# Kernel optimization log

Hardware: AMD Instinct MI355X
Metric: run time of the kernel (lower is better)

Reference implementation:

```python
import jax, jax.numpy as jnp
import numpy as np
import math

B, C, N, M = 4, 128, 4096, 4096

def setup_inputs() -> dict:
    key = jax.random.key(0)
    ks = jax.random.split(key, 8)
    return {
        "x1": jax.random.normal(ks[0], (B, C, N), dtype=jnp.float32),
        "p1": jax.random.normal(ks[1], (B, 3, N), dtype=jnp.float32),
        "x2": jax.random.normal(ks[2], (B, C, M), dtype=jnp.float32),
        "p2": jax.random.normal(ks[3], (B, 3, M), dtype=jnp.float32),
        "Wq": jax.random.normal(ks[4], (C, C), dtype=jnp.float32) * 0.05,
        "Wk": jax.random.normal(ks[5], (C, C), dtype=jnp.float32) * 0.05,
        "Wv": jax.random.normal(ks[6], (C, C), dtype=jnp.float32) * 0.05,
        "Wpos": jax.random.normal(ks[7], (C, 3), dtype=jnp.float32) * 0.05,
    }

def reference(x1, p1, x2, p2, Wq, Wk, Wv, Wpos):
    # Conv1d with kernel_size=1, no bias == per-point matmul over channel dim.
    # NOTE: original forward uses self.pos for BOTH p1 and p2 (pos1 conv unused).
    pos = jnp.einsum('ck,bkn->bcn', Wpos, p1)   # [B,C,N]
    pos1 = jnp.einsum('ck,bkm->bcm', Wpos, p2)  # [B,C,M]
    q = jnp.einsum('dc,bcn->bdn', Wq, x1 + pos)   # [B,C,N]
    k = jnp.einsum('dc,bcm->bdm', Wk, x2 + pos1)  # [B,C,M]
    v = jnp.einsum('dc,bcm->bdm', Wv, x2)         # [B,C,M]
    scale = math.sqrt(q.shape[1])  # sqrt(C) -- q.shape[-2] in (B,C,N) layout
    energy = jnp.einsum('bcn,bcm->bnm', q, k) / scale  # [B,N,M]
    attention = jax.nn.softmax(energy, axis=-1)
    vout = jnp.einsum('bnm,bcm->bnc', attention, v)    # [B,N,C]
    out = jnp.swapaxes(vout, 1, 2) + x1                # [B,C,N] residual
    return jnp.swapaxes(out, 1, 2)                     # [B,N,C]
```

## Files before the change

kernel.cpp:

```cpp
#include <hip/hip_runtime.h>
#include <hip/hip_bf16.h>

#define B_ 4
#define C_ 128
#define N_ 4096
#define M_ 4096

typedef __bf16 bf16;
typedef __bf16 bf16x8 __attribute__((ext_vector_type(8)));
typedef float f32x4 __attribute__((ext_vector_type(4)));
typedef float f32x16 __attribute__((ext_vector_type(16)));

#define MFMA16(a, b, c) __builtin_amdgcn_mfma_f32_16x16x32_bf16(a, b, c, 0, 0, 0)
#define MFMA32(a, b, c) __builtin_amdgcn_mfma_f32_32x32x16_bf16(a, b, c, 0, 0, 0)

__device__ inline void gll16(const bf16* g, bf16* l) {
    __builtin_amdgcn_global_load_lds(
        (const __attribute__((address_space(1))) void*)g,
        (__attribute__((address_space(3))) void*)l, 16, 0, 0);
}

__device__ inline unsigned cvtpk(float a, float b) {
    unsigned r;
    asm("v_cvt_pk_bf16_f32 %0, %1, %2" : "=v"(r) : "v"(a), "v"(b));
    return r;
}

__global__ __launch_bounds__(256) void wcvt_kernel(
    const float* __restrict__ Wq, const float* __restrict__ Wk,
    const float* __restrict__ Wv, bf16* __restrict__ Wb) {
    int i = (blockIdx.x * 256 + threadIdx.x) * 4;
    const float* src = (i < 16384) ? Wq : (i < 32768) ? Wk : Wv;
    int off = i & 16383;
    float4 v = *(const float4*)(src + off);
    union { ushort4 u4; bf16 h[4]; } pk;
    pk.h[0] = (bf16)v.x; pk.h[1] = (bf16)v.y;
    pk.h[2] = (bf16)v.z; pk.h[3] = (bf16)v.w;
    *(ushort4*)(Wb + i) = pk.u4;
}

__global__ __launch_bounds__(256) void proj_kernel(
    const float* __restrict__ x1, const float* __restrict__ p1,
    const float* __restrict__ x2, const float* __restrict__ p2,
    const bf16* __restrict__ Wb, const float* __restrict__ Wpos,
    bf16* __restrict__ Qt, bf16* __restrict__ Kt, bf16* __restrict__ Vt) {
    __shared__ __align__(16) bf16 xt[64 * 136];
    __shared__ float pp[3 * 64], wls[384];

    const int t = threadIdx.x;
    const int b = blockIdx.y;
    const int role = blockIdx.z;
    const int n0 = blockIdx.x * 64;

    const float* xs = (role == 0) ? x1 : x2;
    const float* ps = (role == 0) ? p1 : p2;

    if (role < 2) {
        if (t < 48) {
            int k3 = t / 16, i4 = (t & 15) * 4;
            *(float4*)&pp[k3 * 64 + i4] =
                *(const float4*)(ps + ((size_t)b * 3 + k3) * N_ + n0 + i4);
        } else if (t < 144) {
            int i4 = (t - 48) * 4;
            *(float4*)&wls[i4] = *(const float4*)(Wpos + i4);
        }
    }
    __syncthreads();

    #pragma unroll
    for (int k = 0; k < 8; ++k) {
        int s = t + k * 256;
        int c = s >> 4, n4 = (s & 15) * 4;
        float4 xv = *(const float4*)(xs + ((size_t)b * C_ + c) * N_ + n0 + n4);
        const float* xa = &xv.x;
        if (role < 2) {
            float w0 = wls[c * 3 + 0], w1 = wls[c * 3 + 1], w2 = wls[c * 3 + 2];
            #pragma unroll
            for (int j = 0; j < 4; ++j) {
                float pos = w0 * pp[n4 + j] + w1 * pp[64 + n4 + j] + w2 * pp[128 + n4 + j];
                xt[(n4 + j) * 136 + c] = (bf16)(xa[j] + pos);
            }
        } else {
            #pragma unroll
            for (int j = 0; j < 4; ++j)
                xt[(n4 + j) * 136 + c] = (bf16)xa[j];
        }
    }
    __syncthreads();

    const int w = t >> 6;
    const int lane = t & 63;
    const int col = lane & 15, quad = lane >> 4;
    const int nl = w * 16 + col;

    const bf16* Wm = Wb + role * 16384;

    bf16x8 bx[4];
    #pragma unroll
    for (int cs = 0; cs < 4; ++cs)
        bx[cs] = *(const bf16x8*)&xt[nl * 136 + cs * 32 + quad * 8];

    if (role < 2) {
        bf16* Ot = (role == 0) ? Qt : Kt;
        #pragma unroll
        for (int dt = 0; dt < 8; ++dt) {
            f32x4 acc = {0.f, 0.f, 0.f, 0.f};
            #pragma unroll
            for (int cs = 0; cs < 4; ++cs) {
                bf16x8 wf = *(const bf16x8*)(Wm + (dt * 16 + col) * 128 + cs * 32 + quad * 8);
                acc = MFMA16(bx[cs], wf, acc);
            }
            #pragma unroll
            for (int r = 0; r < 4; ++r) {
                int n = n0 + w * 16 + quad * 4 + r;
                Ot[((size_t)b * N_ + n) * C_ + dt * 16 + col] = (bf16)acc[r];
            }
        }
    } else {
        #pragma unroll
        for (int dt = 0; dt < 8; ++dt) {
            f32x4 acc = {0.f, 0.f, 0.f, 0.f};
            #pragma unroll
            for (int cs = 0; cs < 4; ++cs) {
                bf16x8 wf = *(const bf16x8*)(Wm + (dt * 16 + col) * 128 + cs * 32 + quad * 8);
                acc = MFMA16(wf, bx[cs], acc);
            }
            #pragma unroll
            for (int r = 0; r < 4; ++r)
                Vt[((size_t)b * C_ + dt * 16 + quad * 4 + r) * (size_t)M_ + n0 + nl] = (bf16)acc[r];
        }
    }
}

__global__ __launch_bounds__(512) void attn_kernel(
    const bf16* __restrict__ Qt, const bf16* __restrict__ Kt,
    const bf16* __restrict__ Vt, const float* __restrict__ x1,
    float* __restrict__ out) {
    __shared__ __align__(16) char smem[132096];

    const int t = threadIdx.x;
    const int w = t >> 6;
    const int lane = t & 63;
    const int col = lane & 31;
    const int hi = lane >> 5;
    const int kg = w & 3;
    const int qg = w >> 2;

    const int g0 = blockIdx.x;
    const int xcd = g0 & 7;
    const int b = xcd >> 1;
    const int qt = (xcd & 1) + ((g0 >> 3) << 1);
    const int n0 = qt * 64;

    const float KS = 0.12752107168406815f;

    const bf16* Kbase = Kt + (size_t)b * M_ * C_;
    const bf16* Vbase = Vt + (size_t)b * C_ * M_;

    bf16x8 qf[8];
    {
        const bf16* Qb = Qt + ((size_t)b * N_ + n0 + qg * 32 + col) * C_ + hi * 8;
        #pragma unroll
        for (int cs = 0; cs < 8; ++cs)
            qf[cs] = *(const bf16x8*)(Qb + cs * 16);
    }

    f32x16 oacc[4];
    #pragma unroll
    for (int i = 0; i < 4; ++i)
        #pragma unroll
        for (int j = 0; j < 16; ++j) oacc[i][j] = 0.f;
    float lacc = 0.f;

    const int key_l = (kg << 5) + col;
    const int kxor = (key_l & 15) << 4;

    const bf16* kpp[4];
    const bf16* vpp[4];
    #pragma unroll
    for (int i = 0; i < 4; ++i) {
        int g = ((w << 2) + i) * 64 + lane;
        int row = g >> 4;
        int sp = (g & 15) ^ (row & 15);
        kpp[i] = Kbase + (size_t)row * C_ + sp * 8;
        vpp[i] = Vbase + (size_t)row * M_ + sp * 8;
    }

    auto stageK = [&](char* dst) {
        #pragma unroll
        for (int i = 0; i < 4; ++i) {
            gll16(kpp[i], (bf16*)dst + ((w << 2) + i) * 512);
            kpp[i] += 128 * C_;
        }
    };
    auto stageV = [&](char* dst) {
        #pragma unroll
        for (int i = 0; i < 4; ++i) {
            gll16(vpp[i], (bf16*)dst + ((w << 2) + i) * 512);
            vpp[i] += 128;
        }
    };

    stageK(smem);
    stageV(smem + 65536);
    stageK(smem + 32768);

    f32x16 sA0, sA1, sB0, sB1;

    auto qkc = [&](const char* kbBuf, f32x16& T0, f32x16& T1) {
        #pragma unroll
        for (int q = 0; q < 16; ++q) { T0[q] = 0.f; T1[q] = 0.f; }
        const char* kbp = kbBuf + key_l * 256;
        __builtin_amdgcn_s_setprio(1);
        #pragma unroll
        for (int cs = 0; cs < 4; ++cs) {
            bf16x8 kf = *(const bf16x8*)(kbp + ((((cs << 1) + hi) << 4) ^ kxor));
            T0 = MFMA32(kf, qf[cs], T0);
        }
        #pragma unroll
        for (int cs = 4; cs < 8; ++cs) {
            bf16x8 kf = *(const bf16x8*)(kbp + ((((cs << 1) + hi) << 4) ^ kxor));
            T1 = MFMA32(kf, qf[cs], T1);
        }
        __builtin_amdgcn_s_setprio(0);
    };

    auto smpv = [&](f32x16& S0, f32x16& S1, const char* vbBuf) {
        float p[16];
        #pragma unroll
        for (int r = 0; r < 16; ++r) {
            float e = fminf((S0[r] + S1[r]) * KS, 60.f);
            p[r] = __builtin_amdgcn_exp2f(e);
        }
        {
            float s01 = (p[0] + p[1]) + (p[2] + p[3]);
            float s23 = (p[4] + p[5]) + (p[6] + p[7]);
            float s45 = (p[8] + p[9]) + (p[10] + p[11]);
            float s67 = (p[12] + p[13]) + (p[14] + p[15]);
            lacc += (s01 + s23) + (s45 + s67);
        }
        unsigned W0 = cvtpk(p[0], p[1]),  W1 = cvtpk(p[2], p[3]);
        unsigned W2 = cvtpk(p[4], p[5]),  W3 = cvtpk(p[6], p[7]);
        unsigned W4 = cvtpk(p[8], p[9]),  W5 = cvtpk(p[10], p[11]);
        unsigned W6 = cvtpk(p[12], p[13]), W7 = cvtpk(p[14], p[15]);
        unsigned X0 = hi ? W0 : W2, X1 = hi ? W1 : W3;
        unsigned Y0 = hi ? W4 : W6, Y1 = hi ? W5 : W7;
        X0 = __shfl_xor(X0, 32, 64);  X1 = __shfl_xor(X1, 32, 64);
        Y0 = __shfl_xor(Y0, 32, 64);  Y1 = __shfl_xor(Y1, 32, 64);
        uint4 u0, u1;
        u0.x = hi ? X0 : W0;  u0.y = hi ? X1 : W1;
        u0.z = hi ? W2 : X0;  u0.w = hi ? W3 : X1;
        u1.x = hi ? Y0 : W4;  u1.y = hi ? Y1 : W5;
        u1.z = hi ? W6 : Y0;  u1.w = hi ? W7 : Y1;
        bf16x8 af0 = __builtin_bit_cast(bf16x8, u0);
        bf16x8 af1 = __builtin_bit_cast(bf16x8, u1);

        __builtin_amdgcn_s_setprio(1);
        #pragma unroll
        for (int ct = 0; ct < 4; ++ct) {
            int c = (ct << 5) + col;
            const char* vbp = vbBuf + c * 256;
            int vxor = (c & 15) << 4;
            bf16x8 vf0 = *(const bf16x8*)(vbp + ((((kg << 2) + hi) << 4) ^ vxor));
            bf16x8 vf1 = *(const bf16x8*)(vbp + ((((kg << 2) + 2 + hi) << 4) ^ vxor));
            oacc[ct] = MFMA32(af0, vf0, oacc[ct]);
            oacc[ct] = MFMA32(af1, vf1, oacc[ct]);
        }
        __builtin_amdgcn_s_setprio(0);
    };

    asm volatile("s_waitcnt vmcnt(8)" ::: "memory");
    __builtin_amdgcn_sched_barrier(0);
    __builtin_amdgcn_s_barrier();
    __builtin_amdgcn_sched_barrier(0);
    qkc(smem, sA0, sA1);

    for (int jp = 0; jp < 16; ++jp) {
        const int j0 = jp * 2, j1 = j0 + 1;

        asm volatile("s_waitcnt vmcnt(0)" ::: "memory");
        __builtin_amdgcn_sched_barrier(0);
        __builtin_amdgcn_s_barrier();
        __builtin_amdgcn_sched_barrier(0);
        if (j0 < 31) stageV(smem + 98304);
        if (j0 < 30) stageK(smem);
        if (j0 < 31) qkc(smem + 32768, sB0, sB1);
        smpv(sA0, sA1, smem + 65536);
        asm volatile("s_waitcnt lgkmcnt(0)" ::: "memory");
        __builtin_amdgcn_sched_barrier(0);

        asm volatile("s_waitcnt vmcnt(0)" ::: "memory");
        __builtin_amdgcn_sched_barrier(0);
        __builtin_amdgcn_s_barrier();
        __builtin_amdgcn_sched_barrier(0);
        if (j1 < 31) stageV(smem + 65536);
        if (j1 < 30) stageK(smem + 32768);
        if (j1 < 31) qkc(smem, sA0, sA1);
        smpv(sB0, sB1, smem + 98304);
        asm volatile("s_waitcnt lgkmcnt(0)" ::: "memory");
        __builtin_amdgcn_sched_barrier(0);
    }

    __builtin_amdgcn_s_barrier();

    float* obuf = (float*)smem;
    float* lps  = (float*)(smem + 131072);

    lacc += __shfl_xor(lacc, 32, 64);
    if (hi == 0) lps[(kg << 6) + (qg << 5) + col] = lacc;

    #pragma unroll
    for (int ct = 0; ct < 4; ++ct)
        #pragma unroll
        for (int r = 0; r < 16; ++r) {
            int q = (r & 3) + ((r >> 2) << 3) + (hi << 2);
            obuf[kg * 8192 + ((qg << 5) + q) * 128 + (ct << 5) + col] = oacc[ct][r];
        }
    __syncthreads();

    const int c2 = lane << 1;
    #pragma unroll
    for (int j = 0; j < 8; ++j) {
        int q = (w << 3) + j;
        float s0 = 0.f, s1 = 0.f;
        #pragma unroll
        for (int pp = 0; pp < 4; ++pp) {
            float2 v = *(const float2*)&obuf[pp * 8192 + q * 128 + c2];
            s0 += v.x; s1 += v.y;
        }
        float lsum = lps[q] + lps[64 + q] + lps[128 + q] + lps[192 + q];
        float linv = 1.0f / lsum;
        int n = n0 + q;
        float o0 = s0 * linv + x1[((size_t)b * C_ + c2) * N_ + n];
        float o1 = s1 * linv + x1[((size_t)b * C_ + c2 + 1) * N_ + n];
        *(float2*)&out[((size_t)b * N_ + n) * C_ + c2] = make_float2(o0, o1);
    }
}

extern "C" void kernel_launch(void* const* d_in, const int* in_sizes, int n_in,
                              void* d_out, int out_size, void* d_ws, size_t ws_size,
                              hipStream_t stream) {
    const float* x1   = (const float*)d_in[0];
    const float* p1   = (const float*)d_in[1];
    const float* x2   = (const float*)d_in[2];
    const float* p2   = (const float*)d_in[3];
    const float* Wq   = (const float*)d_in[4];
    const float* Wk   = (const float*)d_in[5];
    const float* Wv   = (const float*)d_in[6];
    const float* Wpos = (const float*)d_in[7];
    float* out = (float*)d_out;

    bf16* Qt = (bf16*)d_ws;
    bf16* Kt = Qt + (size_t)B_ * N_ * C_;
    bf16* Vt = Kt + (size_t)B_ * M_ * C_;

    bf16* Wb = (bf16*)d_out;

    wcvt_kernel<<<dim3(48), dim3(256), 0, stream>>>(Wq, Wk, Wv, Wb);
    proj_kernel<<<dim3(64, B_, 3), dim3(256), 0, stream>>>(
        x1, p1, x2, p2, Wb, Wpos, Qt, Kt, Vt);
    attn_kernel<<<dim3(256), dim3(512), 0, stream>>>(Qt, Kt, Vt, x1, out);
}
```

Measured before the change: 143.8 us.

## Fuse Q projection into attention kernel and merge K/V projection blocks

The Q projection moves into the attention kernel prologue: each block loads its 64 x1 rows, adds the positional term, runs the Wq MFMA into shared memory and reads its Q fragments from there, so the global Q buffer write and read-back go away. K and V projections now share one 512-thread block that loads each x2 tile once and builds both the pos-augmented and raw bf16 copies. The weight buffer moves from the output to the workspace. The cost is a longer attention prologue with extra barriers, plus redundant Wpos and p1 loads in every attention block.

```diff
diff --git a/kernel.cpp b/kernel.cpp
--- a/kernel.cpp
+++ b/kernel.cpp
@@ -39,51 +39,40 @@
     *(ushort4*)(Wb + i) = pk.u4;
 }
 
-__global__ __launch_bounds__(256) void proj_kernel(
-    const float* __restrict__ x1, const float* __restrict__ p1,
+__global__ __launch_bounds__(512) void kvproj_kernel(
     const float* __restrict__ x2, const float* __restrict__ p2,
     const bf16* __restrict__ Wb, const float* __restrict__ Wpos,
-    bf16* __restrict__ Qt, bf16* __restrict__ Kt, bf16* __restrict__ Vt) {
-    __shared__ __align__(16) bf16 xt[64 * 136];
+    bf16* __restrict__ Kt, bf16* __restrict__ Vt) {
+    __shared__ __align__(16) bf16 xp2[64 * 136];
+    __shared__ __align__(16) bf16 xr2[64 * 136];
     __shared__ float pp[3 * 64], wls[384];
 
     const int t = threadIdx.x;
     const int b = blockIdx.y;
-    const int role = blockIdx.z;
     const int n0 = blockIdx.x * 64;
 
-    const float* xs = (role == 0) ? x1 : x2;
-    const float* ps = (role == 0) ? p1 : p2;
-
-    if (role < 2) {
-        if (t < 48) {
-            int k3 = t / 16, i4 = (t & 15) * 4;
-            *(float4*)&pp[k3 * 64 + i4] =
-                *(const float4*)(ps + ((size_t)b * 3 + k3) * N_ + n0 + i4);
-        } else if (t < 144) {
-            int i4 = (t - 48) * 4;
-            *(float4*)&wls[i4] = *(const float4*)(Wpos + i4);
-        }
+    if (t < 48) {
+        int k3 = t / 16, i4 = (t & 15) * 4;
+        *(float4*)&pp[k3 * 64 + i4] =
+            *(const float4*)(p2 + ((size_t)b * 3 + k3) * N_ + n0 + i4);
+    } else if (t < 144) {
+        int i4 = (t - 48) * 4;
+        *(float4*)&wls[i4] = *(const float4*)(Wpos + i4);
     }
     __syncthreads();
 
     #pragma unroll
-    for (int k = 0; k < 8; ++k) {
-        int s = t + k * 256;
+    for (int k = 0; k < 4; ++k) {
+        int s = t + k * 512;
         int c = s >> 4, n4 = (s & 15) * 4;
-        float4 xv = *(const float4*)(xs + ((size_t)b * C_ + c) * N_ + n0 + n4);
+        float4 xv = *(const float4*)(x2 + ((size_t)b * C_ + c) * N_ + n0 + n4);
+        float w0 = wls[c * 3 + 0], w1 = wls[c * 3 + 1], w2 = wls[c * 3 + 2];
         const float* xa = &xv.x;
-        if (role < 2) {
-            float w0 = wls[c * 3 + 0], w1 = wls[c * 3 + 1], w2 = wls[c * 3 + 2];
-            #pragma unroll
-            for (int j = 0; j < 4; ++j) {
-                float pos = w0 * pp[n4 + j] + w1 * pp[64 + n4 + j] + w2 * pp[128 + n4 + j];
-                xt[(n4 + j) * 136 + c] = (bf16)(xa[j] + pos);
-            }
-        } else {
-            #pragma unroll
-            for (int j = 0; j < 4; ++j)
-                xt[(n4 + j) * 136 + c] = (bf16)xa[j];
+        #pragma unroll
+        for (int j = 0; j < 4; ++j) {
+            float pos = w0 * pp[n4 + j] + w1 * pp[64 + n4 + j] + w2 * pp[128 + n4 + j];
+            xp2[(n4 + j) * 136 + c] = (bf16)(xa[j] + pos);
+            xr2[(n4 + j) * 136 + c] = (bf16)xa[j];
         }
     }
     __syncthreads();
@@ -91,17 +80,19 @@
     const int w = t >> 6;
     const int lane = t & 63;
     const int col = lane & 15, quad = lane >> 4;
-    const int nl = w * 16 + col;
-
-    const bf16* Wm = Wb + role * 16384;
+    const int band = w & 3;
+    const int nl = band * 16 + col;
+    const bool isK = (w < 4);
+
+    const bf16* src = isK ? xp2 : xr2;
+    const bf16* Wm = Wb + (isK ? 16384 : 32768);
 
     bf16x8 bx[4];
     #pragma unroll
     for (int cs = 0; cs < 4; ++cs)
-        bx[cs] = *(const bf16x8*)&xt[nl * 136 + cs * 32 + quad * 8];
-
-    if (role < 2) {
-        bf16* Ot = (role == 0) ? Qt : Kt;
+        bx[cs] = *(const bf16x8*)&src[nl * 136 + cs * 32 + quad * 8];
+
+    if (isK) {
         #pragma unroll
         for (int dt = 0; dt < 8; ++dt) {
             f32x4 acc = {0.f, 0.f, 0.f, 0.f};
@@ -112,8 +103,8 @@
             }
             #pragma unroll
             for (int r = 0; r < 4; ++r) {
-                int n = n0 + w * 16 + quad * 4 + r;
-                Ot[((size_t)b * N_ + n) * C_ + dt * 16 + col] = (bf16)acc[r];
+                int n = n0 + band * 16 + quad * 4 + r;
+                Kt[((size_t)b * N_ + n) * C_ + dt * 16 + col] = (bf16)acc[r];
             }
         }
     } else {
@@ -133,8 +124,9 @@
 }
 
 __global__ __launch_bounds__(512) void attn_kernel(
-    const bf16* __restrict__ Qt, const bf16* __restrict__ Kt,
-    const bf16* __restrict__ Vt, const float* __restrict__ x1,
+    const bf16* __restrict__ Kt, const bf16* __restrict__ Vt,
+    const float* __restrict__ x1, const float* __restrict__ p1,
+    const bf16* __restrict__ Wb, const float* __restrict__ Wpos,
     float* __restrict__ out) {
     __shared__ __align__(16) char smem[132096];
 
@@ -157,13 +149,67 @@
     const bf16* Kbase = Kt + (size_t)b * M_ * C_;
     const bf16* Vbase = Vt + (size_t)b * C_ * M_;
 
+    bf16* xq = (bf16*)smem;
+    float* ppq = (float*)(smem + 17408);
+    float* wlsq = (float*)(smem + 18176);
+
+    if (t < 48) {
+        int k3 = t / 16, i4 = (t & 15) * 4;
+        *(float4*)&ppq[k3 * 64 + i4] =
+            *(const float4*)(p1 + ((size_t)b * 3 + k3) * N_ + n0 + i4);
+    } else if (t < 144) {
+        int i4 = (t - 48) * 4;
+        *(float4*)&wlsq[i4] = *(const float4*)(Wpos + i4);
+    }
+    __syncthreads();
+
+    #pragma unroll
+    for (int k = 0; k < 4; ++k) {
+        int s = t + k * 512;
+        int c = s >> 4, n4 = (s & 15) * 4;
+        float4 xv = *(const float4*)(x1 + ((size_t)b * C_ + c) * N_ + n0 + n4);
+        float w0 = wlsq[c * 3 + 0], w1 = wlsq[c * 3 + 1], w2 = wlsq[c * 3 + 2];
+        const float* xa = &xv.x;
+        #pragma unroll
+        for (int j = 0; j < 4; ++j) {
+            float pos = w0 * ppq[n4 + j] + w1 * ppq[64 + n4 + j] + w2 * ppq[128 + n4 + j];
+            xq[(n4 + j) * 136 + c] = (bf16)(xa[j] + pos);
+        }
+    }
+    __syncthreads();
+
+    {
+        const int colq = lane & 15, quadq = lane >> 4;
+        const int nlq = (w & 3) * 16 + colq;
+        bf16x8 bxq[4];
+        #pragma unroll
+        for (int cs = 0; cs < 4; ++cs)
+            bxq[cs] = *(const bf16x8*)&xq[nlq * 136 + cs * 32 + quadq * 8];
+        __syncthreads();
+        const int dt0 = (w >> 2) * 4;
+        #pragma unroll
+        for (int di = 0; di < 4; ++di) {
+            int dt = dt0 + di;
+            f32x4 acc = {0.f, 0.f, 0.f, 0.f};
+            #pragma unroll
+            for (int cs = 0; cs < 4; ++cs) {
+                bf16x8 wf = *(const bf16x8*)(Wb + (dt * 16 + colq) * 128 + cs * 32 + quadq * 8);
+                acc = MFMA16(bxq[cs], wf, acc);
+            }
+            #pragma unroll
+            for (int r = 0; r < 4; ++r)
+                xq[((w & 3) * 16 + quadq * 4 + r) * 136 + dt * 16 + colq] = (bf16)acc[r];
+        }
+        __syncthreads();
+    }
+
     bf16x8 qf[8];
-    {
-        const bf16* Qb = Qt + ((size_t)b * N_ + n0 + qg * 32 + col) * C_ + hi * 8;
-        #pragma unroll
-        for (int cs = 0; cs < 8; ++cs)
-            qf[cs] = *(const bf16x8*)(Qb + cs * 16);
-    }
+    #pragma unroll
+    for (int cs = 0; cs < 8; ++cs)
+        qf[cs] = *(const bf16x8*)&xq[(qg * 32 + col) * 136 + cs * 16 + hi * 8];
+    asm volatile("s_waitcnt lgkmcnt(0)" ::: "memory");
+    __builtin_amdgcn_sched_barrier(0);
+    __builtin_amdgcn_s_barrier();
 
     f32x16 oacc[4];
     #pragma unroll
@@ -350,14 +396,13 @@
     const float* Wpos = (const float*)d_in[7];
     float* out = (float*)d_out;
 
-    bf16* Qt = (bf16*)d_ws;
-    bf16* Kt = Qt + (size_t)B_ * N_ * C_;
+    bf16* Wb = (bf16*)d_ws;
+    bf16* Kt = Wb + 65536;
     bf16* Vt = Kt + (size_t)B_ * M_ * C_;
 
-    bf16* Wb = (bf16*)d_out;
-
     wcvt_kernel<<<dim3(48), dim3(256), 0, stream>>>(Wq, Wk, Wv, Wb);
-    proj_kernel<<<dim3(64, B_, 3), dim3(256), 0, stream>>>(
-        x1, p1, x2, p2, Wb, Wpos, Qt, Kt, Vt);
-    attn_kernel<<<dim3(256), dim3(512), 0, stream>>>(Qt, Kt, Vt, x1, out);
-}
+    kvproj_kernel<<<dim3(64, B_), dim3(512), 0, stream>>>(
+        x2, p2, Wb, Wpos, Kt, Vt);
+    attn_kernel<<<dim3(256), dim3(512), 0, stream>>>(
+        Kt, Vt, x1, p1, Wb, Wpos, out);
+}
```

New measurement: 144.3 us. No clear change (+0.4%).
